# Performance work log

Hardware: AMD Instinct MI355X
Metric: run time of the kernel (lower is better)

Reference implementation:

```python
import jax, jax.numpy as jnp
import numpy as np

B, S, D = 32, 4096, 1024
H = D // 4  # per-branch embedding width


def _lin(k, out_f, in_f):
    # torch nn.Linear default init: U(-1/sqrt(in), 1/sqrt(in))
    kw, kb = jax.random.split(k)
    bound = 1.0 / np.sqrt(in_f)
    W = jax.random.uniform(kw, (out_f, in_f), jnp.float32, -bound, bound)
    b = jax.random.uniform(kb, (out_f,), jnp.float32, -bound, bound)
    return W, b


def setup_inputs() -> dict:
    key = jax.random.key(0)
    kx, kp, kv, ka, kf, ko = jax.random.split(key, 6)
    Wp, bp = _lin(kp, H, 2)
    Wv, bv = _lin(kv, H, 2)
    Wa, ba = _lin(ka, H, 2)
    Wf, bf = _lin(kf, H, 32)
    Wo, bo = _lin(ko, D, D)
    return {
        "pattern": jax.random.normal(kx, (B, S, 2), jnp.float32),
        "Wp": Wp, "bp": bp,
        "Wv": Wv, "bv": bv,
        "Wa": Wa, "ba": ba,
        "Wf": Wf, "bf": bf,
        "Wo": Wo, "bo": bo,
    }


def reference(pattern, Wp, bp, Wv, bv, Wa, ba, Wf, bf, Wo, bo):
    b, s, _ = pattern.shape
    zero = jnp.zeros_like(pattern[:, :1])
    # first-difference velocity / acceleration with zero at t=0
    vel = jnp.concatenate([zero, pattern[:, 1:] - pattern[:, :-1]], axis=1)
    acc = jnp.concatenate([zero, vel[:, 1:] - vel[:, :-1]], axis=1)
    # batched FFT over time axis; keep |first 16 bins| per channel -> [B, 32]
    mag = jnp.abs(jnp.fft.fft(pattern, axis=1))[:, :16, :]  # [B,16,2]
    freq = jnp.concatenate([mag[..., 0], mag[..., 1]], axis=-1)  # [B,32]
    freq = jnp.broadcast_to(freq[:, None, :], (b, s, 32))
    combined = jnp.concatenate([
        pattern @ Wp.T + bp,
        vel @ Wv.T + bv,
        acc @ Wa.T + ba,
        freq @ Wf.T + bf,
    ], axis=-1)  # [B,S,D]
    return combined @ Wo.T + bo
```

## Files before the change

### kernel.cpp

```cpp
#include <hip/hip_runtime.h>

#define BB 32
#define SS 4096
#define DD 1024
#define HH 256

__global__ void k_dft(const float* __restrict__ pat, float* __restrict__ freq) {
    int blk = blockIdx.x;
    int k = blk & 15;
    int c = (blk >> 4) & 1;
    int b = blk >> 5;
    int lane = threadIdx.x;
    const float w = 6.28318530717958647692f / 4096.0f;
    float re = 0.f, im = 0.f;
    for (int t = lane; t < SS; t += 64) {
        float x = pat[(b * SS + t) * 2 + c];
        int m = (k * t) & 4095;
        float ang = w * (float)m;
        re += x * __cosf(ang);
        im += x * __sinf(ang);
    }
    for (int off = 32; off > 0; off >>= 1) {
        re += __shfl_down(re, off);
        im += __shfl_down(im, off);
    }
    if (lane == 0) freq[b * 32 + c * 16 + k] = sqrtf(re * re + im * im);
}

__global__ void k_fwf(const float* __restrict__ freq, const float* __restrict__ Wf,
                      const float* __restrict__ bfv, float* __restrict__ fWf) {
    int b = blockIdx.x;
    int h = threadIdx.x;
    float acc = bfv[h];
    for (int j = 0; j < 32; ++j)
        acc += freq[b * 32 + j] * Wf[h * 32 + j];
    fWf[b * HH + h] = acc;
}

__global__ void k_coef(const float* __restrict__ Wp, const float* __restrict__ Wv,
                       const float* __restrict__ Wa, const float* __restrict__ bp,
                       const float* __restrict__ bv, const float* __restrict__ ba,
                       const float* __restrict__ Wo, const float* __restrict__ bo,
                       float* __restrict__ coef, float* __restrict__ base) {
    int d = blockIdx.x * blockDim.x + threadIdx.x;
    const float* wo = Wo + (size_t)d * DD;
    float mp0 = 0, mp1 = 0, mv0 = 0, mv1 = 0, ma0 = 0, ma1 = 0;
    float bs = bo[d];
    for (int h = 0; h < HH; ++h) {
        float w0 = wo[h];
        float w1 = wo[256 + h];
        float w2 = wo[512 + h];
        mp0 += w0 * Wp[h * 2];  mp1 += w0 * Wp[h * 2 + 1];
        mv0 += w1 * Wv[h * 2];  mv1 += w1 * Wv[h * 2 + 1];
        ma0 += w2 * Wa[h * 2];  ma1 += w2 * Wa[h * 2 + 1];
        bs  += w0 * bp[h] + w1 * bv[h] + w2 * ba[h];
    }
    coef[0 * DD + d] = mp0; coef[1 * DD + d] = mp1;
    coef[2 * DD + d] = mv0; coef[3 * DD + d] = mv1;
    coef[4 * DD + d] = ma0; coef[5 * DD + d] = ma1;
    base[d] = bs;
}

__global__ void k_cb(const float* __restrict__ Wo, const float* __restrict__ fWf,
                     const float* __restrict__ base, float* __restrict__ cb) {
    int idx = blockIdx.x * blockDim.x + threadIdx.x;
    int b = idx >> 10;
    int d = idx & 1023;
    const float* wo = Wo + (size_t)d * DD + 768;
    const float* fw = fWf + b * HH;
    float acc = base[d];
    for (int h = 0; h < HH; ++h) acc += wo[h] * fw[h];
    cb[idx] = acc;
}

__global__ __launch_bounds__(256) void k_main(
        const float2* __restrict__ pat2,
        const float* __restrict__ coef,
        const float* __restrict__ cb,
        float* __restrict__ out) {
    int t = threadIdx.x;
    int d0 = t * 4;
    const int blkPerB = SS / 128;
    int b = blockIdx.x / blkPerB;
    int s0 = (blockIdx.x % blkPerB) * 128;

    float mp0[4], mp1[4], mv0[4], mv1[4], ma0[4], ma1[4], c4[4];
#pragma unroll
    for (int j = 0; j < 4; ++j) {
        mp0[j] = coef[0 * DD + d0 + j];
        mp1[j] = coef[1 * DD + d0 + j];
        mv0[j] = coef[2 * DD + d0 + j];
        mv1[j] = coef[3 * DD + d0 + j];
        ma0[j] = coef[4 * DD + d0 + j];
        ma1[j] = coef[5 * DD + d0 + j];
        c4[j]  = cb[b * DD + d0 + j];
    }
    const float2* prow = pat2 + (size_t)b * SS;
    for (int i = 0; i < 128; ++i) {
        int s = s0 + i;
        float2 P  = prow[s];
        float2 Q  = prow[s >= 1 ? s - 1 : 0];
        float2 R  = prow[s >= 2 ? s - 2 : 0];
        float v0, v1, a0, a1;
        if (s >= 2) {
            v0 = P.x - Q.x; v1 = P.y - Q.y;
            a0 = v0 - (Q.x - R.x); a1 = v1 - (Q.y - R.y);
        } else if (s == 1) {
            v0 = P.x - Q.x; v1 = P.y - Q.y; a0 = v0; a1 = v1;
        } else {
            v0 = 0.f; v1 = 0.f; a0 = 0.f; a1 = 0.f;
        }
        float4 o;
        o.x = c4[0] + P.x * mp0[0] + P.y * mp1[0] + v0 * mv0[0] + v1 * mv1[0] + a0 * ma0[0] + a1 * ma1[0];
        o.y = c4[1] + P.x * mp0[1] + P.y * mp1[1] + v0 * mv0[1] + v1 * mv1[1] + a0 * ma0[1] + a1 * ma1[1];
        o.z = c4[2] + P.x * mp0[2] + P.y * mp1[2] + v0 * mv0[2] + v1 * mv1[2] + a0 * ma0[2] + a1 * ma1[2];
        o.w = c4[3] + P.x * mp0[3] + P.y * mp1[3] + v0 * mv0[3] + v1 * mv1[3] + a0 * ma0[3] + a1 * ma1[3];
        *(float4*)(out + (((size_t)(b * SS + s)) << 10) + d0) = o;
    }
}

extern "C" void kernel_launch(void* const* d_in, const int* in_sizes, int n_in,
                              void* d_out, int out_size, void* d_ws, size_t ws_size,
                              hipStream_t stream) {
    const float* pattern = (const float*)d_in[0];
    const float* Wp = (const float*)d_in[1];
    const float* bp = (const float*)d_in[2];
    const float* Wv = (const float*)d_in[3];
    const float* bv = (const float*)d_in[4];
    const float* Wa = (const float*)d_in[5];
    const float* ba = (const float*)d_in[6];
    const float* Wf = (const float*)d_in[7];
    const float* bfv = (const float*)d_in[8];
    const float* Wo = (const float*)d_in[9];
    const float* bo = (const float*)d_in[10];

    float* ws   = (float*)d_ws;
    float* freq = ws;
    float* fWf  = ws + 1024;
    float* coef = ws + 9216;
    float* base = ws + 15360;
    float* cb   = ws + 16384;
    float* out  = (float*)d_out;

    k_dft <<<1024, 64, 0, stream>>>(pattern, freq);
    k_fwf <<<32, 256, 0, stream>>>(freq, Wf, bfv, fWf);
    k_coef<<<4, 256, 0, stream>>>(Wp, Wv, Wa, bp, bv, ba, Wo, bo, coef, base);
    k_cb  <<<128, 256, 0, stream>>>(Wo, fWf, base, cb);
    k_main<<<1024, 256, 0, stream>>>((const float2*)pattern, coef, cb, out);
}
```

Baseline: 637.2 us.

## Merge prep kernels, parallelize reductions per wavefront, use nontemporal output stores

Fuses the frequency projection and coefficient kernels into one launch. The coefficient and per-batch bias reductions are rebuilt so each wavefront reduces one output with float4 loads and shuffles, which spreads them over far more blocks. The main kernel halves rows per block to double the grid, carries the previous two pattern rows in registers instead of reloading them, and writes the 512MB output with nontemporal stores to limit cache pollution. Prep kernels were a small share of runtime; the output write dominates and stays bandwidth bound.

```diff
diff --git a/kernel.cpp b/kernel.cpp
--- a/kernel.cpp
+++ b/kernel.cpp
@@ -4,6 +4,8 @@
 #define SS 4096
 #define DD 1024
 #define HH 256
+
+typedef float vfloat4 __attribute__((ext_vector_type(4)));
 
 __global__ void k_dft(const float* __restrict__ pat, float* __restrict__ freq) {
     int blk = blockIdx.x;
@@ -27,50 +29,81 @@
     if (lane == 0) freq[b * 32 + c * 16 + k] = sqrtf(re * re + im * im);
 }
 
-__global__ void k_fwf(const float* __restrict__ freq, const float* __restrict__ Wf,
-                      const float* __restrict__ bfv, float* __restrict__ fWf) {
-    int b = blockIdx.x;
-    int h = threadIdx.x;
-    float acc = bfv[h];
-    for (int j = 0; j < 32; ++j)
-        acc += freq[b * 32 + j] * Wf[h * 32 + j];
-    fWf[b * HH + h] = acc;
+__global__ __launch_bounds__(256) void k_fwf_coef(
+        const float* __restrict__ freq, const float* __restrict__ Wf,
+        const float* __restrict__ bfv, float* __restrict__ fWf,
+        const float* __restrict__ Wp, const float* __restrict__ Wv,
+        const float* __restrict__ Wa, const float* __restrict__ bp,
+        const float* __restrict__ bv, const float* __restrict__ ba,
+        const float* __restrict__ Wo, const float* __restrict__ bo,
+        float* __restrict__ coef, float* __restrict__ base) {
+    if (blockIdx.x < 32) {
+        int b = blockIdx.x;
+        int h = threadIdx.x;
+        float acc = bfv[h];
+#pragma unroll
+        for (int j = 0; j < 32; ++j)
+            acc += freq[b * 32 + j] * Wf[h * 32 + j];
+        fWf[b * HH + h] = acc;
+        return;
+    }
+    int d = (blockIdx.x - 32) * 4 + (threadIdx.x >> 6);
+    int lane = threadIdx.x & 63;
+    int h0 = lane * 4;
+    const float* wo = Wo + (size_t)d * DD;
+    float4 w0 = *(const float4*)(wo + h0);
+    float4 w1 = *(const float4*)(wo + 256 + h0);
+    float4 w2 = *(const float4*)(wo + 512 + h0);
+    float4 p0 = *(const float4*)(Wp + h0 * 2);
+    float4 p1 = *(const float4*)(Wp + h0 * 2 + 4);
+    float4 v0 = *(const float4*)(Wv + h0 * 2);
+    float4 v1 = *(const float4*)(Wv + h0 * 2 + 4);
+    float4 a0 = *(const float4*)(Wa + h0 * 2);
+    float4 a1 = *(const float4*)(Wa + h0 * 2 + 4);
+    float4 bpq = *(const float4*)(bp + h0);
+    float4 bvq = *(const float4*)(bv + h0);
+    float4 baq = *(const float4*)(ba + h0);
+
+    float mp0 = w0.x * p0.x + w0.y * p0.z + w0.z * p1.x + w0.w * p1.z;
+    float mp1 = w0.x * p0.y + w0.y * p0.w + w0.z * p1.y + w0.w * p1.w;
+    float mv0 = w1.x * v0.x + w1.y * v0.z + w1.z * v1.x + w1.w * v1.z;
+    float mv1 = w1.x * v0.y + w1.y * v0.w + w1.z * v1.y + w1.w * v1.w;
+    float ma0 = w2.x * a0.x + w2.y * a0.z + w2.z * a1.x + w2.w * a1.z;
+    float ma1 = w2.x * a0.y + w2.y * a0.w + w2.z * a1.y + w2.w * a1.w;
+    float bs  = w0.x * bpq.x + w0.y * bpq.y + w0.z * bpq.z + w0.w * bpq.w
+              + w1.x * bvq.x + w1.y * bvq.y + w1.z * bvq.z + w1.w * bvq.w
+              + w2.x * baq.x + w2.y * baq.y + w2.z * baq.z + w2.w * baq.w;
+
+    for (int off = 32; off > 0; off >>= 1) {
+        mp0 += __shfl_down(mp0, off);
+        mp1 += __shfl_down(mp1, off);
+        mv0 += __shfl_down(mv0, off);
+        mv1 += __shfl_down(mv1, off);
+        ma0 += __shfl_down(ma0, off);
+        ma1 += __shfl_down(ma1, off);
+        bs  += __shfl_down(bs,  off);
+    }
+    if (lane == 0) {
+        coef[0 * DD + d] = mp0; coef[1 * DD + d] = mp1;
+        coef[2 * DD + d] = mv0; coef[3 * DD + d] = mv1;
+        coef[4 * DD + d] = ma0; coef[5 * DD + d] = ma1;
+        base[d] = bo[d] + bs;
+    }
 }
 
-__global__ void k_coef(const float* __restrict__ Wp, const float* __restrict__ Wv,
-                       const float* __restrict__ Wa, const float* __restrict__ bp,
-                       const float* __restrict__ bv, const float* __restrict__ ba,
-                       const float* __restrict__ Wo, const float* __restrict__ bo,
-                       float* __restrict__ coef, float* __restrict__ base) {
-    int d = blockIdx.x * blockDim.x + threadIdx.x;
-    const float* wo = Wo + (size_t)d * DD;
-    float mp0 = 0, mp1 = 0, mv0 = 0, mv1 = 0, ma0 = 0, ma1 = 0;
-    float bs = bo[d];
-    for (int h = 0; h < HH; ++h) {
-        float w0 = wo[h];
-        float w1 = wo[256 + h];
-        float w2 = wo[512 + h];
-        mp0 += w0 * Wp[h * 2];  mp1 += w0 * Wp[h * 2 + 1];
-        mv0 += w1 * Wv[h * 2];  mv1 += w1 * Wv[h * 2 + 1];
-        ma0 += w2 * Wa[h * 2];  ma1 += w2 * Wa[h * 2 + 1];
-        bs  += w0 * bp[h] + w1 * bv[h] + w2 * ba[h];
-    }
-    coef[0 * DD + d] = mp0; coef[1 * DD + d] = mp1;
-    coef[2 * DD + d] = mv0; coef[3 * DD + d] = mv1;
-    coef[4 * DD + d] = ma0; coef[5 * DD + d] = ma1;
-    base[d] = bs;
-}
-
-__global__ void k_cb(const float* __restrict__ Wo, const float* __restrict__ fWf,
-                     const float* __restrict__ base, float* __restrict__ cb) {
-    int idx = blockIdx.x * blockDim.x + threadIdx.x;
-    int b = idx >> 10;
-    int d = idx & 1023;
-    const float* wo = Wo + (size_t)d * DD + 768;
-    const float* fw = fWf + b * HH;
-    float acc = base[d];
-    for (int h = 0; h < HH; ++h) acc += wo[h] * fw[h];
-    cb[idx] = acc;
+__global__ __launch_bounds__(256) void k_cb(
+        const float* __restrict__ Wo, const float* __restrict__ fWf,
+        const float* __restrict__ base, float* __restrict__ cb) {
+    int wid = blockIdx.x * 4 + (threadIdx.x >> 6);
+    int lane = threadIdx.x & 63;
+    int b = wid >> 10;
+    int d = wid & 1023;
+    int h0 = lane * 4;
+    float4 w = *(const float4*)(Wo + (size_t)d * DD + 768 + h0);
+    float4 f = *(const float4*)(fWf + b * HH + h0);
+    float acc = w.x * f.x + w.y * f.y + w.z * f.z + w.w * f.w;
+    for (int off = 32; off > 0; off >>= 1) acc += __shfl_down(acc, off);
+    if (lane == 0) cb[wid] = base[d] + acc;
 }
 
 __global__ __launch_bounds__(256) void k_main(
@@ -80,9 +113,10 @@
         float* __restrict__ out) {
     int t = threadIdx.x;
     int d0 = t * 4;
-    const int blkPerB = SS / 128;
+    const int ROWS = 64;
+    const int blkPerB = SS / ROWS;
     int b = blockIdx.x / blkPerB;
-    int s0 = (blockIdx.x % blkPerB) * 128;
+    int s0 = (blockIdx.x % blkPerB) * ROWS;
 
     float mp0[4], mp1[4], mv0[4], mv1[4], ma0[4], ma1[4], c4[4];
 #pragma unroll
@@ -96,11 +130,13 @@
         c4[j]  = cb[b * DD + d0 + j];
     }
     const float2* prow = pat2 + (size_t)b * SS;
-    for (int i = 0; i < 128; ++i) {
+    float2 Q, R;
+    if (s0 >= 2) { Q = prow[s0 - 1]; R = prow[s0 - 2]; }
+    else         { Q = prow[0];      R = prow[0]; }
+
+    for (int i = 0; i < ROWS; ++i) {
         int s = s0 + i;
-        float2 P  = prow[s];
-        float2 Q  = prow[s >= 1 ? s - 1 : 0];
-        float2 R  = prow[s >= 2 ? s - 2 : 0];
+        float2 P = prow[s];
         float v0, v1, a0, a1;
         if (s >= 2) {
             v0 = P.x - Q.x; v1 = P.y - Q.y;
@@ -110,12 +146,13 @@
         } else {
             v0 = 0.f; v1 = 0.f; a0 = 0.f; a1 = 0.f;
         }
-        float4 o;
+        vfloat4 o;
         o.x = c4[0] + P.x * mp0[0] + P.y * mp1[0] + v0 * mv0[0] + v1 * mv1[0] + a0 * ma0[0] + a1 * ma1[0];
         o.y = c4[1] + P.x * mp0[1] + P.y * mp1[1] + v0 * mv0[1] + v1 * mv1[1] + a0 * ma0[1] + a1 * ma1[1];
         o.z = c4[2] + P.x * mp0[2] + P.y * mp1[2] + v0 * mv0[2] + v1 * mv1[2] + a0 * ma0[2] + a1 * ma1[2];
         o.w = c4[3] + P.x * mp0[3] + P.y * mp1[3] + v0 * mv0[3] + v1 * mv1[3] + a0 * ma0[3] + a1 * ma1[3];
-        *(float4*)(out + (((size_t)(b * SS + s)) << 10) + d0) = o;
+        __builtin_nontemporal_store(o, (vfloat4*)(out + (((size_t)(b * SS + s)) << 10) + d0));
+        R = Q; Q = P;
     }
 }
 
@@ -142,9 +179,9 @@
     float* cb   = ws + 16384;
     float* out  = (float*)d_out;
 
-    k_dft <<<1024, 64, 0, stream>>>(pattern, freq);
-    k_fwf <<<32, 256, 0, stream>>>(freq, Wf, bfv, fWf);
-    k_coef<<<4, 256, 0, stream>>>(Wp, Wv, Wa, bp, bv, ba, Wo, bo, coef, base);
-    k_cb  <<<128, 256, 0, stream>>>(Wo, fWf, base, cb);
-    k_main<<<1024, 256, 0, stream>>>((const float2*)pattern, coef, cb, out);
+    k_dft     <<<1024, 64, 0, stream>>>(pattern, freq);
+    k_fwf_coef<<<288, 256, 0, stream>>>(freq, Wf, bfv, fWf,
+                                        Wp, Wv, Wa, bp, bv, ba, Wo, bo, coef, base);
+    k_cb      <<<8192, 256, 0, stream>>>(Wo, fWf, base, cb);
+    k_main    <<<2048, 256, 0, stream>>>((const float2*)pattern, coef, cb, out);
 }
```

Result: faster. 578.8 us (-9.2%).
